# Performance work log

Hardware: AMD Instinct MI355X
Metric: run time of the kernel (lower is better)

## Reference

```python
import jax, jax.numpy as jnp
from jax import lax
import numpy as np

B, CB, HW, HID, P, NC = 128, 200, 32, 32, 4, 10
DEPTH, D, DI, DS, DR, K = 4, 128, 256, 16, 8, 4
G = HW // P                  # 8 -> 64 spatial patches
SPA_N = G * G
SPE_N = CB // 2              # 100 spectral patches
HS, HE = HW // 2 - 5 // 2, HW // 2 + 5 // 2 + 1   # centered 5x5 spectral crop: 14:19


def _sincos_1d(d, pos):
    omega = 1.0 / 10000 ** (np.arange(d // 2, dtype=np.float64) / (d / 2.0))
    out = np.outer(pos.reshape(-1).astype(np.float64), omega)
    return np.concatenate([np.sin(out), np.cos(out)], axis=1)


def _spa_pos_embed():
    # MAE get_2d_sincos_pos_embed with cls_token=True (zeros row FIRST)
    gw, gh = np.meshgrid(np.arange(G, dtype=np.float64), np.arange(G, dtype=np.float64))
    emb = np.concatenate([_sincos_1d(D // 2, gw), _sincos_1d(D // 2, gh)], axis=1)
    return np.concatenate([np.zeros((1, D)), emb], axis=0)  # (SPA_N+1, D)


def _spe_pos_embed():
    pe = np.zeros((SPE_N + 1, D))
    pos = np.arange(SPE_N + 1, dtype=np.float64)[:, None]
    div = np.exp(np.arange(0, D, 2) * -(np.log(10000.0) / D))
    pe[:, 0::2] = np.sin(pos * div)
    pe[:, 1::2] = np.cos(pos * div)
    return pe


def setup_inputs():
    keys = iter(jax.random.split(jax.random.key(0), 64))
    r = lambda shape, s=0.02: jax.random.normal(next(keys), shape, jnp.float32) * s
    return dict(
        x=jax.random.normal(next(keys), (B, CB, HW, HW), jnp.float32),
        spa_pos=jnp.asarray(_spa_pos_embed(), jnp.float32),
        spe_pos=jnp.asarray(_spe_pos_embed(), jnp.float32),
        dr_w1=r((HID, CB)), dr_b1=r((HID,)), bn1_g=1.0 + r((HID,)), bn1_b=r((HID,)),
        dr_w2=r((HID, HID)), dr_b2=r((HID,)), bn2_g=1.0 + r((HID,)), bn2_b=r((HID,)),
        spa_pw=r((D, HID, P, P)), spa_pb=r((D,)),
        spe_pw=r((D, 25, 2)), spe_pb=r((D,)),
        spa_cls=r((1, 1, D)), spe_cls=r((1, 1, D)),
        ln_g=jnp.ones((DEPTH, 2, D), jnp.float32), ln_b=jnp.zeros((DEPTH, 2, D), jnp.float32),
        in_w=r((DEPTH, 2, 2 * DI, D)),
        conv_w=r((DEPTH, 2, DI, K), 0.2), conv_b=r((DEPTH, 2, DI)),
        xp_w=r((DEPTH, 2, DR + 2 * DS, DI)),
        dtp_w=r((DEPTH, 2, DI, DR), 0.1), dtp_b=r((DEPTH, 2, DI), 0.1),
        a_log=jnp.log(jnp.tile(jnp.arange(1.0, DS + 1.0, dtype=jnp.float32), (DEPTH, 2, DI, 1))),
        d_p=jnp.ones((DEPTH, 2, DI), jnp.float32),
        out_w=r((DEPTH, 2, D, DI)),
        l1_w=r((DEPTH, D, D)),
        head_w=r((NC, D)), head_b=r((NC,)),
    )


def _layernorm(x, g, b, eps=1e-6):
    m = x.mean(-1, keepdims=True)
    v = jnp.mean((x - m) ** 2, axis=-1, keepdims=True)
    return (x - m) * lax.rsqrt(v + eps) * g + b


def _batchnorm(x, g, b, eps=1e-5):
    # training-mode BN: biased batch stats over (B,H,W) per channel
    m = x.mean((0, 2, 3), keepdims=True)
    v = x.var((0, 2, 3), keepdims=True)
    return (x - m) * lax.rsqrt(v + eps) * g[None, :, None, None] + b[None, :, None, None]


def _ssm(x, in_w, cw, cb, xpw, dtw, dtb, alog, dpar, ow):
    # standard Mamba selective-scan block (expand=2, d_conv=4)
    Bb, L, _ = x.shape
    xz = jnp.einsum('bld,ed->ble', x, in_w)
    xc, z = jnp.split(xz, 2, axis=-1)
    xt = jnp.pad(xc.transpose(0, 2, 1), ((0, 0), (0, 0), (K - 1, 0)))  # causal pad
    xt = lax.conv_general_dilated(xt, cw[:, None, :], (1,), 'VALID', feature_group_count=DI)
    xc = jax.nn.silu(xt + cb[None, :, None]).transpose(0, 2, 1)        # (B,L,DI)
    dbl = jnp.einsum('bld,ed->ble', xc, xpw)
    dt = jax.nn.softplus(jnp.einsum('blr,dr->bld', dbl[..., :DR], dtw) + dtb)
    Bm, Cm = dbl[..., DR:DR + DS], dbl[..., DR + DS:]
    dA = jnp.exp(dt[..., None] * (-jnp.exp(alog)))                     # (B,L,DI,DS)
    dBx = (dt * xc)[..., None] * Bm[:, :, None, :]                     # (B,L,DI,DS)

    def step(h, ab):
        h = ab[0] * h + ab[1]
        return h, h

    _, hs = lax.scan(step, jnp.zeros((Bb, DI, DS), xc.dtype),
                     (dA.transpose(1, 0, 2, 3), dBx.transpose(1, 0, 2, 3)))
    y = jnp.einsum('lbds,bls->bld', hs, Cm) + xc * dpar
    return jnp.einsum('bld,ed->ble', y * jax.nn.silu(z), ow)


def _block(inp, lg, lb, sp):
    # block_1D: bidirectional SSM with trailing cls token kept in place
    xn = _layernorm(inp, lg, lb)
    x1 = _ssm(xn, *sp)
    x2 = jnp.concatenate([xn[:, :-1][:, ::-1], xn[:, -1:]], axis=1)
    x3 = _ssm(x2, *sp)
    x3 = jnp.concatenate([x3[:, :-1][:, ::-1], x3[:, -1:]], axis=1)
    return (x1 + x3) * 0.5 + inp


def reference(x, spa_pos, spe_pos, dr_w1, dr_b1, bn1_g, bn1_b, dr_w2, dr_b2, bn2_g, bn2_b,
              spa_pw, spa_pb, spe_pw, spe_pb, spa_cls, spe_cls, ln_g, ln_b, in_w, conv_w,
              conv_b, xp_w, dtp_w, dtp_b, a_log, d_p, out_w, l1_w, head_w, head_b):
    Bb = x.shape[0]
    # dimen_redu: 1x1 conv -> BN -> ReLU -> 1x1 conv -> BN
    h = jnp.einsum('bchw,oc->bohw', x, dr_w1) + dr_b1[None, :, None, None]
    h = jax.nn.relu(_batchnorm(h, bn1_g, bn1_b))
    h = jnp.einsum('bchw,oc->bohw', h, dr_w2) + dr_b2[None, :, None, None]
    h = _batchnorm(h, bn2_g, bn2_b)
    # spatial patch embed (conv k=stride=P == patchify + matmul)
    hr = h.reshape(Bb, HID, G, P, G, P)
    x_spa = jnp.einsum('bcipjq,dcpq->bijd', hr, spa_pw).reshape(Bb, SPA_N, D) + spa_pb
    x_spa = x_spa + spa_pos[None, :-1, :]
    x_spa = jnp.concatenate([x_spa, jnp.broadcast_to(spa_cls + spa_pos[None, -1:, :], (Bb, 1, D))], axis=1)
    # spectral patch embed on centered 5x5 crop: Conv1d(25->D, k=stride=2) over bands
    xc = x[:, :, HS:HE, HS:HE].reshape(Bb, CB, 25).transpose(0, 2, 1).reshape(Bb, 25, SPE_N, 2)
    x_spe = jnp.einsum('bcls,dcs->bld', xc, spe_pw) + spe_pb
    x_spe = x_spe + spe_pos[None, :-1, :]
    x_spe = jnp.concatenate([x_spe, jnp.broadcast_to(spe_cls + spe_pos[None, -1:, :], (Bb, 1, D))], axis=1)
    for i in range(DEPTH):
        spa_p = (in_w[i, 0], conv_w[i, 0], conv_b[i, 0], xp_w[i, 0], dtp_w[i, 0], dtp_b[i, 0], a_log[i, 0], d_p[i, 0], out_w[i, 0])
        spe_p = (in_w[i, 1], conv_w[i, 1], conv_b[i, 1], xp_w[i, 1], dtp_w[i, 1], dtp_b[i, 1], a_log[i, 1], d_p[i, 1], out_w[i, 1])
        x_spa = _block(x_spa, ln_g[i, 0], ln_b[i, 0], spa_p)
        x_spe = _block(x_spe, ln_g[i, 1], ln_b[i, 1], spe_p)
        # sigmoid-gated fusion (fu=True)
        c = (x_spa[:, (x_spa.shape[1] - 1) // 2, :] + x_spe.mean(axis=1)) * 0.5
        sig = jax.nn.sigmoid(c @ l1_w[i].T)[:, None, :]
        x_spa = x_spa * sig
        x_spe = x_spe * sig
    out = (x_spa[:, -1] + x_spe[:, -1]) * 0.5   # cls tokens (global_pool=False)
    return out @ head_w.T + head_b
```

## Files before the change

### kernel.cpp

```cpp
#include <hip/hip_runtime.h>
#include <math.h>

typedef float4 f4;
typedef __attribute__((ext_vector_type(8))) short short8v;
typedef __attribute__((ext_vector_type(4))) float f32x4;
typedef __attribute__((ext_vector_type(2))) float f32x2;

constexpr int B_ = 128, CB_ = 200, HW_ = 32, HID_ = 32, D_ = 128, DI_ = 256;
constexpr int DS_ = 16, DR_ = 8, KC_ = 4, DEPTH_ = 4, NC_ = 10;
constexpr int LSPA_ = 65, LSPE_ = 101, NPIX_ = 1024;
constexpr int M1_ = B_ * NPIX_;
constexpr int NWI_ = DEPTH_*2*512*D_;
constexpr int NWO_ = DEPTH_*2*D_*DI_;
constexpr int NWX_ = DEPTH_*2*40*DI_;
constexpr int NWTR_ = 65536;

constexpr size_t O_XSPA = 0;
constexpr size_t O_XSPE = O_XSPA + (size_t)B_*LSPA_*D_;
constexpr size_t O_SC   = O_XSPE + (size_t)B_*LSPE_*D_;
constexpr size_t O_BN1P = O_SC + 512;
constexpr size_t O_BN2P = O_BN1P + 512*64;
constexpr size_t O_U    = O_BN2P + 512*64;
constexpr size_t O_HP1  = O_U;
constexpr size_t O_HP2  = O_U + (size_t)M1_*HID_;
constexpr size_t O_WTR  = O_HP2 + (size_t)M1_*HID_;
constexpr size_t O_XZSPA = O_U;
constexpr size_t O_XZSPE = O_XZSPA + (size_t)B_*LSPA_*512;
constexpr size_t O_XCSPA = O_XZSPE + (size_t)B_*LSPE_*512;
constexpr size_t O_XCSPE = O_XCSPA + (size_t)2*B_*LSPA_*DI_;
constexpr size_t O_DBSPA = O_XCSPE + (size_t)2*B_*LSPE_*DI_;
constexpr size_t O_DBSPE = O_DBSPA + (size_t)2*B_*LSPA_*40;
constexpr size_t O_YZSPA = O_DBSPE + (size_t)2*B_*LSPE_*40;
constexpr size_t O_YZSPE = O_YZSPA + (size_t)2*B_*LSPA_*DI_;
constexpr size_t O_WHI_I = O_YZSPE + (size_t)2*B_*LSPE_*DI_;
constexpr size_t O_WLO_I = O_WHI_I + NWI_/2;
constexpr size_t O_WHI_O = O_WLO_I + NWI_/2;
constexpr size_t O_WLO_O = O_WHI_O + NWO_/2;
constexpr size_t O_WHI_X = O_WLO_O + NWO_/2;
constexpr size_t O_WLO_X = O_WHI_X + NWX_/2;

static __device__ __forceinline__ unsigned short f2bf(float f) {
    unsigned int u = __float_as_uint(f);
    unsigned int r = u + 0x7fffu + ((u >> 16) & 1u);
    return (unsigned short)(r >> 16);
}
static __device__ __forceinline__ float bf2f(unsigned short h) {
    return __uint_as_float(((unsigned int)h) << 16);
}

__global__ __launch_bounds__(256) void k_stem1(const float* __restrict__ x,
        const float* __restrict__ w1, const float* __restrict__ b1,
        float* __restrict__ hpre1, float* __restrict__ part)
{
    __shared__ float smem[8448];
    float* sw = smem;
    const int t = threadIdx.x;
    for (int i = t; i < CB_*HID_; i += 256) {
        int c = i >> 5, o = i & 31;
        sw[i] = w1[o*CB_ + c];
    }
    const int m = blockIdx.x*256 + t;
    const int b = m >> 10, pix = m & 1023;
    const float* xp = x + (size_t)b*CB_*NPIX_ + pix;
    float h[HID_];
    #pragma unroll
    for (int o = 0; o < HID_; o++) h[o] = b1[o];
    __syncthreads();
    for (int c8 = 0; c8 < CB_; c8 += 8) {
        float xv[8];
        #pragma unroll
        for (int j = 0; j < 8; j++) xv[j] = xp[(size_t)(c8 + j)*NPIX_];
        #pragma unroll
        for (int j = 0; j < 8; j++) {
            const f4* wr = (const f4*)(sw + (c8 + j)*HID_);
            #pragma unroll
            for (int o8 = 0; o8 < 8; o8++) {
                f4 wv = wr[o8];
                h[o8*4+0] = fmaf(xv[j], wv.x, h[o8*4+0]);
                h[o8*4+1] = fmaf(xv[j], wv.y, h[o8*4+1]);
                h[o8*4+2] = fmaf(xv[j], wv.z, h[o8*4+2]);
                h[o8*4+3] = fmaf(xv[j], wv.w, h[o8*4+3]);
            }
        }
    }
    f4* hp = (f4*)(hpre1 + (size_t)m*HID_);
    #pragma unroll
    for (int o = 0; o < HID_; o += 4) { f4 v = {h[o],h[o+1],h[o+2],h[o+3]}; hp[o>>2] = v; }
    __syncthreads();
    float* sred = smem;
    #pragma unroll
    for (int o = 0; o < HID_; o++) sred[t*33 + o] = h[o];
    __syncthreads();
    if (t < HID_) {
        float s = 0.f, q = 0.f;
        for (int j = 0; j < 256; j++) { float v = sred[j*33 + t]; s += v; q += v*v; }
        part[blockIdx.x*64 + t]      = s;
        part[blockIdx.x*64 + 32 + t] = q;
    }
}

__global__ void k_bnfix(const float* __restrict__ part, const float* __restrict__ g,
        const float* __restrict__ bta, float* __restrict__ scale, float* __restrict__ shift)
{
    const int o = threadIdx.x;
    if (o >= 32) return;
    float s = 0.f, q = 0.f;
    for (int j = 0; j < 512; j++) { s += part[j*64 + o]; q += part[j*64 + 32 + o]; }
    const float mean = s / (float)M1_;
    const float var  = q / (float)M1_ - mean*mean;
    const float sc = g[o] * rsqrtf(var + 1e-5f);
    scale[o] = sc;
    shift[o] = bta[o] - mean*sc;
}

__global__ void k_bnfix_spa(const float* __restrict__ part, const float* __restrict__ g,
        const float* __restrict__ bta, const float* __restrict__ spa_pw,
        const float* __restrict__ spa_pb, float* __restrict__ scale,
        float* __restrict__ shift, float* __restrict__ spa_shift)
{
    __shared__ float ssh[32];
    const int t = threadIdx.x;
    if (t < 32) {
        float s = 0.f, q = 0.f;
        for (int j = 0; j < 512; j++) { s += part[j*64 + t]; q += part[j*64 + 32 + t]; }
        const float mean = s / (float)M1_;
        const float var  = q / (float)M1_ - mean*mean;
        const float sc = g[t] * rsqrtf(var + 1e-5f);
        scale[t] = sc;
        const float sh = bta[t] - mean*sc;
        shift[t] = sh;
        ssh[t] = sh;
    }
    __syncthreads();
    float acc = spa_pb[t];
    for (int c = 0; c < HID_; c++) {
        float wsum = 0.f;
        #pragma unroll
        for (int pq = 0; pq < 16; pq++) wsum += spa_pw[((size_t)t*HID_ + c)*16 + pq];
        acc = fmaf(ssh[c], wsum, acc);
    }
    spa_shift[t] = acc;
}

__global__ __launch_bounds__(256) void k_stem2(const float* __restrict__ hpre1,
        const float* __restrict__ w2, const float* __restrict__ b2,
        const float* __restrict__ sc1, const float* __restrict__ sh1,
        float* __restrict__ hpre2, float* __restrict__ part)
{
    __shared__ float smem[8448];
    __shared__ float s_sc[HID_], s_sh[HID_], s_b2[HID_];
    float* sw = smem;
    const int t = threadIdx.x;
    for (int i = t; i < HID_*HID_; i += 256) {
        int c = i >> 5, o = i & 31;
        sw[i] = w2[o*HID_ + c];
    }
    if (t < HID_) { s_sc[t] = sc1[t]; s_sh[t] = sh1[t]; s_b2[t] = b2[t]; }
    __syncthreads();
    const int m = blockIdx.x*256 + t;
    const f4* hp = (const f4*)(hpre1 + (size_t)m*HID_);
    float a[HID_];
    #pragma unroll
    for (int c = 0; c < HID_; c += 4) { f4 v = hp[c>>2]; a[c]=v.x; a[c+1]=v.y; a[c+2]=v.z; a[c+3]=v.w; }
    #pragma unroll
    for (int c = 0; c < HID_; c++) a[c] = fmaxf(fmaf(a[c], s_sc[c], s_sh[c]), 0.f);
    float h[HID_];
    #pragma unroll
    for (int o = 0; o < HID_; o++) h[o] = s_b2[o];
    #pragma unroll
    for (int c = 0; c < HID_; c++) {
        const f4* wr = (const f4*)(sw + c*HID_);
        #pragma unroll
        for (int o8 = 0; o8 < 8; o8++) {
            f4 wv = wr[o8];
            h[o8*4+0] = fmaf(a[c], wv.x, h[o8*4+0]);
            h[o8*4+1] = fmaf(a[c], wv.y, h[o8*4+1]);
            h[o8*4+2] = fmaf(a[c], wv.z, h[o8*4+2]);
            h[o8*4+3] = fmaf(a[c], wv.w, h[o8*4+3]);
        }
    }
    f4* op = (f4*)(hpre2 + (size_t)m*HID_);
    #pragma unroll
    for (int o = 0; o < HID_; o += 4) { f4 v = {h[o],h[o+1],h[o+2],h[o+3]}; op[o>>2] = v; }
    __syncthreads();
    float* sred = smem;
    #pragma unroll
    for (int o = 0; o < HID_; o++) sred[t*33 + o] = h[o];
    __syncthreads();
    if (t < HID_) {
        float s = 0.f, q = 0.f;
// ... 46 lines not shown
    for (int i = 0; i < 2; i++)
        #pragma unroll
        for (int j = 0; j < 8; j++) acc[i][j] = 0.f;
    for (int pq = 0; pq < 16; pq++) {
        const int p = pq >> 2, q = pq & 3;
        __syncthreads();
        for (int idx = t; idx < 32*8; idx += 256) {
            const int n = idx >> 3, c4 = (idx & 7)*4;
            const int nn = n0 + n;
            const int ii = nn >> 3, jj = nn & 7;
            const int pix = (ii*4 + p)*HW_ + jj*4 + q;
            f4 v = *(const f4*)(hpre2 + ((size_t)b*NPIX_ + pix)*HID_ + c4);
            float* pp = &sA[n*36 + c4];
            pp[0] = v.x*s_sc[c4]; pp[1] = v.y*s_sc[c4+1]; pp[2] = v.z*s_sc[c4+2]; pp[3] = v.w*s_sc[c4+3];
        }
        for (int idx = t; idx < 128*8; idx += 256) {
            const int dd = idx >> 3, c4 = (idx & 7)*4;
            f4 v = *(const f4*)(wtr + pq*4096 + dd*HID_ + c4);
            float* pp = &sB[dd*36 + c4];
            pp[0]=v.x; pp[1]=v.y; pp[2]=v.z; pp[3]=v.w;
        }
        __syncthreads();
        #pragma unroll
        for (int kq = 0; kq < 8; kq++) {
            f4 a0 = *(const f4*)&sA[(ty*2+0)*36 + kq*4];
            f4 a1 = *(const f4*)&sA[(ty*2+1)*36 + kq*4];
            #pragma unroll
            for (int j = 0; j < 8; j++) {
                const f4 bv = *(const f4*)&sB[(tx + 16*j)*36 + kq*4];
                acc[0][j] = fmaf(a0.x,bv.x,fmaf(a0.y,bv.y,fmaf(a0.z,bv.z,fmaf(a0.w,bv.w,acc[0][j]))));
                acc[1][j] = fmaf(a1.x,bv.x,fmaf(a1.y,bv.y,fmaf(a1.z,bv.z,fmaf(a1.w,bv.w,acc[1][j]))));
            }
        }
    }
    #pragma unroll
    for (int i = 0; i < 2; i++) {
        const int n = n0 + ty*2 + i;
        float* orow = xspa + ((size_t)b*LSPA_ + n)*D_;
        #pragma unroll
        for (int j = 0; j < 8; j++) {
            const int d = tx + 16*j;
            orow[d] = acc[i][j] + spa_shift[d] + spa_pos[n*D_ + d];
        }
    }
    if (half == 0 && t < D_)
        xspa[((size_t)b*LSPA_ + 64)*D_ + t] = spa_cls[t] + spa_pos[64*D_ + t];
}

__global__ __launch_bounds__(256) void k_spe(const float* __restrict__ x,
        const float* __restrict__ spe_pw, const float* __restrict__ spe_pb,
        const float* __restrict__ spe_pos, const float* __restrict__ spe_cls,
        float* __restrict__ xspe)
{
    const int b = blockIdx.x >> 1, half = blockIdx.x & 1;
    __shared__ float sx[100*25];
    __shared__ float sw[D_*51];
    const int t = threadIdx.x;
    for (int idx = t; idx < 100*25; idx += 256) {
        const int ch = idx / 25 + half*100, c = idx % 25;
        sx[idx] = x[(size_t)b*CB_*NPIX_ + (size_t)ch*NPIX_ + (14 + c/5)*HW_ + 14 + c%5];
    }
    for (int idx = t; idx < D_*50; idx += 256) sw[(idx/50)*51 + idx%50] = spe_pw[idx];
    __syncthreads();
    const int d = t & 127, ls = t >> 7;
    for (int j = ls; j < 50; j += 2) {
        const int l = half*50 + j;
        float acc = spe_pb[d];
        const float* wr = sw + d*51;
        const float* xr = sx + (2*j)*25;
        #pragma unroll
        for (int c = 0; c < 25; c++) {
            acc = fmaf(xr[c],      wr[c*2],     acc);
            acc = fmaf(xr[25 + c], wr[c*2 + 1], acc);
        }
        xspe[((size_t)b*LSPE_ + l)*D_ + d] = acc + spe_pos[l*D_ + d];
    }
    if (half == 1 && t < D_)
        xspe[((size_t)b*LSPE_ + 100)*D_ + t] = spe_cls[t] + spe_pos[100*D_ + t];
}

__global__ __launch_bounds__(256) void k_ln_in(const float* __restrict__ xspa,
        const float* __restrict__ xspe, float* __restrict__ xz_spa, float* __restrict__ xz_spe,
        const unsigned short* __restrict__ whi, const unsigned short* __restrict__ wlo,
        const float* __restrict__ ln_g, const float* __restrict__ ln_b, int depth)
{
    const int br = blockIdx.z;
    const int L = br ? LSPE_ : LSPA_;
    const int M = B_ * L;
    const int m0 = blockIdx.x*64;
    if (m0 >= M) return;
    const float* X  = br ? xspe : xspa;
    float* XZ = br ? xz_spe : xz_spa;
    const size_t wb = ((size_t)depth*2 + br) * 512 * (size_t)D_;
    const unsigned short* WH = whi + wb;
    const unsigned short* WL = wlo + wb;
    const float* gg = ln_g + ((size_t)depth*2 + br)*D_;
    const float* bb = ln_b + ((size_t)depth*2 + br)*D_;

    __shared__ __align__(16) unsigned short sAhi[64*136];
    __shared__ __align__(16) unsigned short sAlo[64*136];
    __shared__ __align__(16) unsigned short sBhi[128*40];
    __shared__ __align__(16) unsigned short sBlo[128*40];
    __shared__ float sgb[256];

    const int t = threadIdx.x;
    sgb[t] = (t < 128) ? gg[t] : bb[t-128];

    {
        const int row = t >> 2, tq = t & 3;
        const float* xr = X + (size_t)(m0 + row)*D_ + tq*32;
        float v[32];
        #pragma unroll
        for (int j4 = 0; j4 < 8; j4++) {
            f4 u = *(const f4*)(xr + j4*4);
            v[j4*4] = u.x; v[j4*4+1] = u.y; v[j4*4+2] = u.z; v[j4*4+3] = u.w;
        }
        float s = 0.f, q = 0.f;
        #pragma unroll
        for (int j = 0; j < 32; j++) { s += v[j]; q += v[j]*v[j]; }
        s += __shfl_xor(s, 1); q += __shfl_xor(q, 1);
        s += __shfl_xor(s, 2); q += __shfl_xor(q, 2);
        const float mean = s * (1.f/128.f);
        const float rstd = rsqrtf(q*(1.f/128.f) - mean*mean + 1e-6f);
        __syncthreads();
        unsigned short uh[32], ul[32];
        #pragma unroll
        for (int j = 0; j < 32; j++) {
            const int k = tq*32 + j;
            const float w = (v[j] - mean)*rstd*sgb[k] + sgb[128 + k];
            const unsigned short h = f2bf(w);
            uh[j] = h;
            ul[j] = f2bf(w - bf2f(h));
        }
        #pragma unroll
        for (int j4 = 0; j4 < 8; j4++) {
            ushort4 a = {uh[j4*4], uh[j4*4+1], uh[j4*4+2], uh[j4*4+3]};
            ushort4 b = {ul[j4*4], ul[j4*4+1], ul[j4*4+2], ul[j4*4+3]};
            *(ushort4*)&sAhi[row*136 + tq*32 + j4*4] = a;
            *(ushort4*)&sAlo[row*136 + tq*32 + j4*4] = b;
        }
    }
    __syncthreads();

    const int n0 = blockIdx.y * 128;
    const int wv = t >> 6, l = t & 63;
    const int wm = wv >> 1, wn = wv & 1;
    const int lr = l & 15, lg = l >> 4;
    f32x4 acc[2][4];
    #pragma unroll
    for (int i = 0; i < 2; i++)
        #pragma unroll
        for (int j = 0; j < 4; j++) acc[i][j] = (f32x4){0.f,0.f,0.f,0.f};

    for (int kc = 0; kc < 4; kc++) {
        {
            const int n = t >> 1, off = (t & 1)*16;
            const size_t g = (size_t)(n0 + n)*D_ + kc*32 + off;
            const uint4* ph = (const uint4*)(WH + g);
            const uint4* pl = (const uint4*)(WL + g);
            uint4 h0 = ph[0], h1 = ph[1];
            uint4 l0 = pl[0], l1 = pl[1];
            uint4* dh = (uint4*)&sBhi[n*40 + off];
            uint4* dl = (uint4*)&sBlo[n*40 + off];
            dh[0] = h0; dh[1] = h1;
            dl[0] = l0; dl[1] = l1;
        }
        __syncthreads();
        short8v ah[2], al[2], bh[4], bl[4];
        #pragma unroll
        for (int i = 0; i < 2; i++) {
            const int ro = (wm*32 + i*16 + lr)*136 + kc*32 + lg*8;
            ah[i] = *(const short8v*)&sAhi[ro];
            al[i] = *(const short8v*)&sAlo[ro];
        }
        #pragma unroll
        for (int j = 0; j < 4; j++) {
            const int co = (wn*64 + j*16 + lr)*40 + lg*8;
            bh[j] = *(const short8v*)&sBhi[co];
            bl[j] = *(const short8v*)&sBlo[co];
        }
        #pragma unroll
        for (int i = 0; i < 2; i++)
            #pragma unroll
            for (int j = 0; j < 4; j++) {
                acc[i][j] = __builtin_amdgcn_mfma_f32_16x16x32_bf16(ah[i], bh[j], acc[i][j], 0, 0, 0);
                acc[i][j] = __builtin_amdgcn_mfma_f32_16x16x32_bf16(ah[i], bl[j], acc[i][j], 0, 0, 0);
                acc[i][j] = __builtin_amdgcn_mfma_f32_16x16x32_bf16(al[i], bh[j], acc[i][j], 0, 0, 0);
            }
        __syncthreads();
    }

    #pragma unroll
    for (int i = 0; i < 2; i++) {
        const int rbase = m0 + wm*32 + i*16 + lg*4;
        #pragma unroll
        for (int j = 0; j < 4; j++) {
            const int col = n0 + wn*64 + j*16 + lr;
            #pragma unroll
            for (int r = 0; r < 4; r++)
                XZ[(size_t)(rbase + r)*512 + col] = acc[i][j][r];
        }
    }
}

__global__ __launch_bounds__(256) void k_conv(const float* __restrict__ xz_spa,
        const float* __restrict__ xz_spe, float* __restrict__ xc_spa, float* __restrict__ xc_spe,
        const float* __restrict__ conv_w, const float* __restrict__ conv_b, int depth)
{
    const int br = blockIdx.z;
    const int L = br ? LSPE_ : LSPA_;
    const int nt = (L + 15) / 16;
    const int b = blockIdx.x % B_;
    const int tl = blockIdx.x / B_;
    if (tl >= nt) return;
    const int l0 = tl * 16;
    const int d = threadIdx.x;
    const float* XZ = (br ? xz_spe : xz_spa) + (size_t)b*L*512 + d;
    float* XC0 = (br ? xc_spe : xc_spa) + ((size_t)(0*B_ + b)*L)*DI_ + d;
    float* XC1 = (br ? xc_spe : xc_spa) + ((size_t)(1*B_ + b)*L)*DI_ + d;
    const size_t w = (size_t)depth*2 + br;
    const float* cw = conv_w + (w*DI_ + d)*KC_;
    const float cb = conv_b[w*DI_ + d];
// ... 184 lines not shown
    _Pragma("unroll")                                                         \
    for (int c_ = 0; c_ < 8; ++c_) {                                          \
        const int l_ = (J0) + c_;                                             \
        if (l_ < L) {                                                         \
            const float* dr = &sD[BUF][c_*40];                                \
            const f4 q0 = *(const f4*)(dr);                                   \
            const f4 q1 = *(const f4*)(dr + 4);                               \
            f32x2 r2 = (f32x2){q0.x,q0.y} * dtw2[0];                          \
            r2 = __builtin_elementwise_fma((f32x2){q0.z,q0.w}, dtw2[1], r2);  \
            r2 = __builtin_elementwise_fma((f32x2){q1.x,q1.y}, dtw2[2], r2);  \
            r2 = __builtin_elementwise_fma((f32x2){q1.z,q1.w}, dtw2[3], r2);  \
            const float raw = dtb + r2.x + r2.y;                              \
            const float er = __builtin_amdgcn_exp2f(raw * 1.4426950408889634f);\
            const float dt = (raw > 20.f) ? raw                               \
                : __log2f(1.f + er) * 0.6931471805599453f;                    \
            const float xcv = RX[c_], zv = RZ[c_];                            \
            const float c2 = dt * xcv;                                        \
            const float E1 = __builtin_amdgcn_exp2f(nA0 * dt);                \
            const float E2 = E1 * E1;                                         \
            const f4 B0=*(const f4*)(dr+8),  B1=*(const f4*)(dr+12);          \
            const f4 B2=*(const f4*)(dr+16), B3=*(const f4*)(dr+20);          \
            const f4 C0=*(const f4*)(dr+24), C1=*(const f4*)(dr+28);          \
            const f4 C2=*(const f4*)(dr+32), C3=*(const f4*)(dr+36);          \
            const f32x2 Bp[8] = {{B0.x,B0.y},{B0.z,B0.w},{B1.x,B1.y},{B1.z,B1.w},\
                                 {B2.x,B2.y},{B2.z,B2.w},{B3.x,B3.y},{B3.z,B3.w}};\
            const f32x2 Cp[8] = {{C0.x,C0.y},{C0.z,C0.w},{C1.x,C1.y},{C1.z,C1.w},\
                                 {C2.x,C2.y},{C2.z,C2.w},{C3.x,C3.y},{C3.z,C3.w}};\
            f32x2 e = (f32x2){E1, E2};                                        \
            const f32x2 estep = (f32x2){E2, E2};                              \
            const f32x2 c2v = (f32x2){c2, c2};                                \
            f32x2 y2 = (f32x2){0.f, 0.f};                                     \
            _Pragma("unroll")                                                 \
            for (int j_ = 0; j_ < 8; ++j_) {                                  \
                h2[j_] = __builtin_elementwise_fma(h2[j_], e, c2v*Bp[j_]);    \
                y2 = __builtin_elementwise_fma(h2[j_], Cp[j_], y2);           \
                e = e * estep;                                                \
            }                                                                 \
            const float y = y2.x + y2.y;                                      \
            const float yt = fmaf(xcv, dpv, y);                               \
            const float sg = __builtin_amdgcn_rcpf(                           \
                1.f + __builtin_amdgcn_exp2f(-zv * 1.4426950408889634f));     \
            const int ls_ = dir ? ((l_ == L-1) ? (L-1) : (L-2-l_)) : l_;      \
            YZ[(size_t)ls_*DI_ + t] = yt * (zv * sg);                         \
        }                                                                     \
    }                                                                         \
} while(0)

    const int nch = (L + 7) >> 3;
    LOADD(0);
    LOADX(0, rxA, rzA);
    WRITED(0);
    __syncthreads();
    int ck = 0;
    while (true) {
        {
            const int j0 = ck*8;
            const bool more = (ck + 1 < nch);
            if (more) { LOADD(j0 + 8); LOADX(j0 + 8, rxB, rzB); }
            SCAN_CHUNK(j0, 0, rxA, rzA);
            if (more) WRITED(1);
            __syncthreads();
            if (!more) break;
            ck++;
        }
        {
            const int j0 = ck*8;
            const bool more = (ck + 1 < nch);
            if (more) { LOADD(j0 + 8); LOADX(j0 + 8, rxA, rzA); }
            SCAN_CHUNK(j0, 1, rxB, rzB);
            if (more) WRITED(0);
            __syncthreads();
            if (!more) break;
            ck++;
        }
    }
#undef LOADD
#undef WRITED
#undef LOADX
#undef SCAN_CHUNK
}

__global__ __launch_bounds__(256) void k_out(float* __restrict__ xspa, float* __restrict__ xspe,
        const float* __restrict__ yz_spa, const float* __restrict__ yz_spe,
        const unsigned short* __restrict__ whiO, const unsigned short* __restrict__ wloO, int depth)
{
    const int br = blockIdx.z;
    const int L = br ? LSPE_ : LSPA_;
    const int M = B_ * L;
    const int m0 = blockIdx.x*64;
    if (m0 >= M) return;
    float* X = br ? xspe : xspa;
    const float* Y0 = br ? yz_spe : yz_spa;
    const float* Y1 = Y0 + (size_t)B_*L*DI_;
    const size_t wb = ((size_t)depth*2 + br) * (size_t)D_ * DI_;
    const unsigned short* WH = whiO + wb;
    const unsigned short* WL = wloO + wb;

    __shared__ __align__(16) unsigned short sAhi[64*40];
    __shared__ __align__(16) unsigned short sAlo[64*40];
    __shared__ __align__(16) unsigned short sBhi[128*40];
    __shared__ __align__(16) unsigned short sBlo[128*40];

    const int t = threadIdx.x;
    const int wv = t >> 6, l = t & 63;
    const int wm = wv >> 1, wn = wv & 1;
    const int lr = l & 15, lg = l >> 4;
    f32x4 acc[2][4];
    #pragma unroll
    for (int i = 0; i < 2; i++)
        #pragma unroll
        for (int j = 0; j < 4; j++) acc[i][j] = (f32x4){0.f,0.f,0.f,0.f};

    for (int kc = 0; kc < 8; kc++) {
        {
            const int r = t >> 2, q = t & 3;
            const size_t g = (size_t)(m0 + r)*DI_ + kc*32 + q*8;
            unsigned short uh[8], ul[8];
            #pragma unroll
            for (int j4 = 0; j4 < 2; j4++) {
                f4 u0 = *(const f4*)(Y0 + g + j4*4);
                f4 u1 = *(const f4*)(Y1 + g + j4*4);
                float vv[4] = {u0.x+u1.x, u0.y+u1.y, u0.z+u1.z, u0.w+u1.w};
                #pragma unroll
                for (int e = 0; e < 4; e++) {
                    const unsigned short hh = f2bf(vv[e]);
                    uh[j4*4+e] = hh;
                    ul[j4*4+e] = f2bf(vv[e] - bf2f(hh));
                }
            }
            #pragma unroll
            for (int j4 = 0; j4 < 2; j4++) {
                ushort4 a = {uh[j4*4], uh[j4*4+1], uh[j4*4+2], uh[j4*4+3]};
                ushort4 b = {ul[j4*4], ul[j4*4+1], ul[j4*4+2], ul[j4*4+3]};
                *(ushort4*)&sAhi[r*40 + q*8 + j4*4] = a;
                *(ushort4*)&sAlo[r*40 + q*8 + j4*4] = b;
            }
            const int n = t >> 1, off = (t & 1)*16;
            const size_t gb = (size_t)n*DI_ + kc*32 + off;
            uint4 h0 = *(const uint4*)(WH + gb);
            uint4 h1 = *(const uint4*)(WH + gb + 8);
            uint4 l0 = *(const uint4*)(WL + gb);
            uint4 l1 = *(const uint4*)(WL + gb + 8);
            uint4* dh = (uint4*)&sBhi[n*40 + off];
            uint4* dl = (uint4*)&sBlo[n*40 + off];
            dh[0] = h0; dh[1] = h1;
            dl[0] = l0; dl[1] = l1;
        }
        __syncthreads();
        short8v ah[2], al[2], bh[4], bl[4];
        #pragma unroll
        for (int i = 0; i < 2; i++) {
            const int ro = (wm*32 + i*16 + lr)*40 + lg*8;
            ah[i] = *(const short8v*)&sAhi[ro];
            al[i] = *(const short8v*)&sAlo[ro];
        }
        #pragma unroll
        for (int j = 0; j < 4; j++) {
            const int co = (wn*64 + j*16 + lr)*40 + lg*8;
            bh[j] = *(const short8v*)&sBhi[co];
            bl[j] = *(const short8v*)&sBlo[co];
        }
        #pragma unroll
        for (int i = 0; i < 2; i++)
            #pragma unroll
            for (int j = 0; j < 4; j++) {
                acc[i][j] = __builtin_amdgcn_mfma_f32_16x16x32_bf16(ah[i], bh[j], acc[i][j], 0, 0, 0);
                acc[i][j] = __builtin_amdgcn_mfma_f32_16x16x32_bf16(ah[i], bl[j], acc[i][j], 0, 0, 0);
                acc[i][j] = __builtin_amdgcn_mfma_f32_16x16x32_bf16(al[i], bh[j], acc[i][j], 0, 0, 0);
            }
        __syncthreads();
    }

    #pragma unroll
    for (int i = 0; i < 2; i++) {
        const int rbase = m0 + wm*32 + i*16 + lg*4;
        #pragma unroll
        for (int j = 0; j < 4; j++) {
            const int col = wn*64 + j*16 + lr;
            #pragma unroll
            for (int r = 0; r < 4; r++)
                X[(size_t)(rbase + r)*D_ + col] += 0.5f*acc[i][j][r];
        }
    }
}

__global__ __launch_bounds__(256) void k_gate(float* __restrict__ xspa,
        float* __restrict__ xspe, const float* __restrict__ l1_w, int depth)
{
    __shared__ float sp[2][128];
    __shared__ float sc[128];
    __shared__ float sduo[256];
    __shared__ __align__(16) float ss[128];
    const int b = blockIdx.x, t = threadIdx.x;
    const int dd = t & 127, rh = t >> 7;
    float s = 0.f;
    for (int l = rh; l < LSPE_; l += 2) s += xspe[((size_t)b*LSPE_ + l)*D_ + dd];
    sp[rh][dd] = s;
    __syncthreads();
    if (t < 128)
        sc[t] = 0.5f*(xspa[((size_t)b*LSPA_ + 32)*D_ + t] + (sp[0][t]+sp[1][t])*(1.f/101.f));
    __syncthreads();
    {
        const float* wr = l1_w + (size_t)depth*D_*D_ + (size_t)dd*D_ + rh*64;
        float acc = 0.f;
        #pragma unroll 4
        for (int k = 0; k < 64; k++) acc = fmaf(sc[rh*64 + k], wr[k], acc);
        sduo[t] = acc;
    }
    __syncthreads();
    if (t < 128)
        ss[t] = 1.f/(1.f + __expf(-(sduo[t] + sduo[t+128])));
    __syncthreads();
    f4* pa = (f4*)(xspa + (size_t)b*LSPA_*D_);
    for (int idx = t; idx < LSPA_*32; idx += 256) {
        const f4 sg = *((const f4*)ss + (idx & 31));
        f4 v = pa[idx];
        v.x *= sg.x; v.y *= sg.y; v.z *= sg.z; v.w *= sg.w;
        pa[idx] = v;
    }
    f4* pe = (f4*)(xspe + (size_t)b*LSPE_*D_);
    for (int idx = t; idx < LSPE_*32; idx += 256) {
        const f4 sg = *((const f4*)ss + (idx & 31));
        f4 v = pe[idx];
        v.x *= sg.x; v.y *= sg.y; v.z *= sg.z; v.w *= sg.w;
        pe[idx] = v;
    }
}

__global__ void k_head(const float* __restrict__ xspa, const float* __restrict__ xspe,
        const float* __restrict__ head_w, const float* __restrict__ head_b, float* __restrict__ out)
{
    __shared__ float sv[D_];
    const int b = blockIdx.x, t = threadIdx.x;
    if (t < D_) sv[t] = 0.5f*(xspa[((size_t)b*LSPA_ + 64)*D_ + t] + xspe[((size_t)b*LSPE_ + 100)*D_ + t]);
    __syncthreads();
    if (t < NC_) {
        float acc = head_b[t];
        for (int k = 0; k < D_; k++) acc = fmaf(sv[k], head_w[t*D_ + k], acc);
        out[b*NC_ + t] = acc;
    }
}

extern "C" void kernel_launch(void* const* d_in, const int* in_sizes, int n_in,
                              void* d_out, int out_size, void* d_ws, size_t ws_size,
                              hipStream_t stream)
{
    const float* x       = (const float*)d_in[0];
    const float* spa_pos = (const float*)d_in[1];
    const float* spe_pos = (const float*)d_in[2];
    const float* dr_w1   = (const float*)d_in[3];
    const float* dr_b1   = (const float*)d_in[4];
    const float* bn1_g   = (const float*)d_in[5];
    const float* bn1_b   = (const float*)d_in[6];
    const float* dr_w2   = (const float*)d_in[7];
    const float* dr_b2   = (const float*)d_in[8];
    const float* bn2_g   = (const float*)d_in[9];
    const float* bn2_b   = (const float*)d_in[10];
    const float* spa_pw  = (const float*)d_in[11];
    const float* spa_pb  = (const float*)d_in[12];
    const float* spe_pw  = (const float*)d_in[13];
    const float* spe_pb  = (const float*)d_in[14];
    const float* spa_cls = (const float*)d_in[15];
    const float* spe_cls = (const float*)d_in[16];
    const float* ln_g    = (const float*)d_in[17];
    const float* ln_b    = (const float*)d_in[18];
    const float* in_w    = (const float*)d_in[19];
    const float* conv_w  = (const float*)d_in[20];
    const float* conv_b  = (const float*)d_in[21];
    const float* xp_w    = (const float*)d_in[22];
    const float* dtp_w   = (const float*)d_in[23];
    const float* dtp_b   = (const float*)d_in[24];
    const float* a_log   = (const float*)d_in[25];
    const float* d_p     = (const float*)d_in[26];
    const float* out_w   = (const float*)d_in[27];
    const float* l1_w    = (const float*)d_in[28];
    const float* head_w  = (const float*)d_in[29];
    const float* head_b  = (const float*)d_in[30];

    float* ws = (float*)d_ws;
    float* xspa   = ws + O_XSPA;
    float* xspe   = ws + O_XSPE;
    float* scale1 = ws + O_SC;
    float* shift1 = ws + O_SC + 32;
    float* scale2 = ws + O_SC + 64;
    float* shift2 = ws + O_SC + 96;
    float* spa_sh = ws + O_SC + 128;
    float* bn1p   = ws + O_BN1P;
    float* bn2p   = ws + O_BN2P;
    float* hpre1  = ws + O_HP1;
    float* hpre2  = ws + O_HP2;
    float* wtr    = ws + O_WTR;
    float* xz_spa = ws + O_XZSPA;
    float* xz_spe = ws + O_XZSPE;
    float* xc_spa = ws + O_XCSPA;
    float* xc_spe = ws + O_XCSPE;
    float* db_spa = ws + O_DBSPA;
    float* db_spe = ws + O_DBSPE;
    float* yz_spa = ws + O_YZSPA;
    float* yz_spe = ws + O_YZSPE;
    unsigned short* whiI = (unsigned short*)(ws + O_WHI_I);
    unsigned short* wloI = (unsigned short*)(ws + O_WLO_I);
    unsigned short* whiO = (unsigned short*)(ws + O_WHI_O);
    unsigned short* wloO = (unsigned short*)(ws + O_WLO_O);
    unsigned short* whiX = (unsigned short*)(ws + O_WHI_X);
    unsigned short* wloX = (unsigned short*)(ws + O_WLO_X);

    hipLaunchKernelGGL(k_stem1, dim3(512), dim3(256), 0, stream, x, dr_w1, dr_b1, hpre1, bn1p);
    hipLaunchKernelGGL(k_bnfix, dim3(1), dim3(32), 0, stream, bn1p, bn1_g, bn1_b, scale1, shift1);
    hipLaunchKernelGGL(k_wsplit, dim3((NWI_+NWO_+NWX_+NWTR_+255)/256), dim3(256), 0, stream,
                       in_w, out_w, xp_w, spa_pw, whiI, wloI, whiO, wloO, whiX, wloX, wtr);
    hipLaunchKernelGGL(k_stem2, dim3(512), dim3(256), 0, stream, hpre1, dr_w2, dr_b2, scale1, shift1, hpre2, bn2p);
    hipLaunchKernelGGL(k_bnfix_spa, dim3(1), dim3(128), 0, stream, bn2p, bn2_g, bn2_b,
                       spa_pw, spa_pb, scale2, shift2, spa_sh);
    hipLaunchKernelGGL(k_patch, dim3(256), dim3(256), 0, stream, hpre2, wtr, scale2, spa_sh, spa_pos, spa_cls, xspa);
    hipLaunchKernelGGL(k_spe, dim3(256), dim3(256), 0, stream, x, spe_pw, spe_pb, spe_pos, spe_cls, xspe);

    for (int i = 0; i < DEPTH_; i++) {
        hipLaunchKernelGGL(k_ln_in, dim3(202, 4, 2), dim3(256), 0, stream,
                           xspa, xspe, xz_spa, xz_spe, whiI, wloI, ln_g, ln_b, i);
        hipLaunchKernelGGL(k_conv, dim3(B_*7, 1, 2), dim3(256), 0, stream,
                           xz_spa, xz_spe, xc_spa, xc_spe, conv_w, conv_b, i);
        hipLaunchKernelGGL(k_xp, dim3(202, 1, 2), dim3(256), 0, stream,
                           xc_spa, xc_spe, db_spa, db_spe, whiX, wloX, i);
        hipLaunchKernelGGL(k_scan, dim3(B_, 2, 2), dim3(256), 0, stream,
                           xz_spa, xz_spe, xc_spa, xc_spe, db_spa, db_spe,
                           yz_spa, yz_spe, a_log, dtp_w, dtp_b, d_p, i);
        hipLaunchKernelGGL(k_out, dim3(202, 1, 2), dim3(256), 0, stream,
                           xspa, xspe, yz_spa, yz_spe, whiO, wloO, i);
        hipLaunchKernelGGL(k_gate, dim3(128), dim3(256), 0, stream, xspa, xspe, l1_w, i);
    }
    hipLaunchKernelGGL(k_head, dim3(128), dim3(128), 0, stream,
                       xspa, xspe, head_w, head_b, (float*)d_out);
}
```

Before: 711.9 us.

## Use split-bf16 MFMA in stem GEMM and fold sigmoid gating into consumers

The first stem 1x1-conv GEMM moves from per-thread fp32 FMAs to MFMA bf16 hi/lo split products. It now uses 128-row tiles and twice as many blocks, with a two-level in-block BN partial reduction. The per-depth gate kernel no longer rescales the whole spatial and spectral activations. It only writes the sigmoid vector, and the scale is applied lazily where the activations are next read: the LN/in-proj prologue, the out-proj residual update, and the head. This removes a full read-modify-write pass over the activations per depth and raises matrix throughput in the stem. In exchange it adds per-row division to find the batch index and slightly reduces precision in the stem GEMM.

```diff
diff --git a/kernel.cpp b/kernel.cpp
--- a/kernel.cpp
+++ b/kernel.cpp
@@ -19,7 +19,7 @@
 constexpr size_t O_XSPE = O_XSPA + (size_t)B_*LSPA_*D_;
 constexpr size_t O_SC   = O_XSPE + (size_t)B_*LSPE_*D_;
 constexpr size_t O_BN1P = O_SC + 512;
-constexpr size_t O_BN2P = O_BN1P + 512*64;
+constexpr size_t O_BN2P = O_BN1P + 1024*64;
 constexpr size_t O_U    = O_BN2P + 512*64;
 constexpr size_t O_HP1  = O_U;
 constexpr size_t O_HP2  = O_U + (size_t)M1_*HID_;
@@ -52,48 +52,108 @@
         const float* __restrict__ w1, const float* __restrict__ b1,
         float* __restrict__ hpre1, float* __restrict__ part)
 {
-    __shared__ float smem[8448];
-    float* sw = smem;
+    __shared__ __align__(16) unsigned char smem[25600];
+    unsigned short* sAhi = (unsigned short*)smem;
+    unsigned short* sAlo = (unsigned short*)(smem + 10240);
+    unsigned short* sBhi = (unsigned short*)(smem + 20480);
+    unsigned short* sBlo = (unsigned short*)(smem + 23040);
     const int t = threadIdx.x;
-    for (int i = t; i < CB_*HID_; i += 256) {
-        int c = i >> 5, o = i & 31;
-        sw[i] = w1[o*CB_ + c];
-    }
-    const int m = blockIdx.x*256 + t;
-    const int b = m >> 10, pix = m & 1023;
-    const float* xp = x + (size_t)b*CB_*NPIX_ + pix;
-    float h[HID_];
-    #pragma unroll
-    for (int o = 0; o < HID_; o++) h[o] = b1[o];
-    __syncthreads();
-    for (int c8 = 0; c8 < CB_; c8 += 8) {
-        float xv[8];
-        #pragma unroll
-        for (int j = 0; j < 8; j++) xv[j] = xp[(size_t)(c8 + j)*NPIX_];
-        #pragma unroll
-        for (int j = 0; j < 8; j++) {
-            const f4* wr = (const f4*)(sw + (c8 + j)*HID_);
-            #pragma unroll
-            for (int o8 = 0; o8 < 8; o8++) {
-                f4 wv = wr[o8];
-                h[o8*4+0] = fmaf(xv[j], wv.x, h[o8*4+0]);
-                h[o8*4+1] = fmaf(xv[j], wv.y, h[o8*4+1]);
-                h[o8*4+2] = fmaf(xv[j], wv.z, h[o8*4+2]);
-                h[o8*4+3] = fmaf(xv[j], wv.w, h[o8*4+3]);
-            }
-        }
-    }
-    f4* hp = (f4*)(hpre1 + (size_t)m*HID_);
-    #pragma unroll
-    for (int o = 0; o < HID_; o += 4) { f4 v = {h[o],h[o+1],h[o+2],h[o+3]}; hp[o>>2] = v; }
-    __syncthreads();
-    float* sred = smem;
-    #pragma unroll
-    for (int o = 0; o < HID_; o++) sred[t*33 + o] = h[o];
-    __syncthreads();
-    if (t < HID_) {
+    const int m0 = blockIdx.x * 128;
+    const int b = m0 >> 10, pix0 = m0 & 1023;
+    const float* xb = x + (size_t)b*CB_*NPIX_ + pix0;
+    const int wv = t >> 6, l = t & 63;
+    const int lr = l & 15, lg = l >> 4;
+    f32x4 acc[2][2];
+    #pragma unroll
+    for (int i = 0; i < 2; i++)
+        #pragma unroll
+        for (int j = 0; j < 2; j++) acc[i][j] = (f32x4){0.f,0.f,0.f,0.f};
+
+    const int rA = t >> 1, khA = (t & 1)*16;
+    for (int kc = 0; kc < 7; kc++) {
+        {
+            unsigned short uh[16], ul[16];
+            #pragma unroll
+            for (int j = 0; j < 16; j++) {
+                const int k = kc*32 + khA + j;
+                const float v = (k < CB_) ? xb[(size_t)k*NPIX_ + rA] : 0.f;
+                const unsigned short h = f2bf(v);
+                uh[j] = h; ul[j] = f2bf(v - bf2f(h));
+            }
+            #pragma unroll
+            for (int j4 = 0; j4 < 4; j4++) {
+                ushort4 a = {uh[j4*4], uh[j4*4+1], uh[j4*4+2], uh[j4*4+3]};
+                ushort4 c = {ul[j4*4], ul[j4*4+1], ul[j4*4+2], ul[j4*4+3]};
+                *(ushort4*)&sAhi[rA*40 + khA + j4*4] = a;
+                *(ushort4*)&sAlo[rA*40 + khA + j4*4] = c;
+            }
+            for (int idx = t; idx < 32*32; idx += 256) {
+                const int n = idx >> 5, kk = idx & 31;
+                const int k = kc*32 + kk;
+                const float v = (k < CB_) ? w1[n*CB_ + k] : 0.f;
+                const unsigned short h = f2bf(v);
+                sBhi[n*40 + kk] = h;
+                sBlo[n*40 + kk] = f2bf(v - bf2f(h));
+            }
+        }
+        __syncthreads();
+        short8v ah[2], al[2], bh[2], bl[2];
+        #pragma unroll
+        for (int i = 0; i < 2; i++) {
+            const int ro = (wv*32 + i*16 + lr)*40 + lg*8;
+            ah[i] = *(const short8v*)&sAhi[ro];
+            al[i] = *(const short8v*)&sAlo[ro];
+        }
+        #pragma unroll
+        for (int j = 0; j < 2; j++) {
+            const int co = (j*16 + lr)*40 + lg*8;
+            bh[j] = *(const short8v*)&sBhi[co];
+            bl[j] = *(const short8v*)&sBlo[co];
+        }
+        #pragma unroll
+        for (int i = 0; i < 2; i++)
+            #pragma unroll
+            for (int j = 0; j < 2; j++) {
+                acc[i][j] = __builtin_amdgcn_mfma_f32_16x16x32_bf16(ah[i], bh[j], acc[i][j], 0, 0, 0);
+                acc[i][j] = __builtin_amdgcn_mfma_f32_16x16x32_bf16(ah[i], bl[j], acc[i][j], 0, 0, 0);
+                acc[i][j] = __builtin_amdgcn_mfma_f32_16x16x32_bf16(al[i], bh[j], acc[i][j], 0, 0, 0);
+            }
+        __syncthreads();
+    }
+
+    float* sred = (float*)smem;
+    float* scomb = (float*)(smem + 20480);
+    #pragma unroll
+    for (int i = 0; i < 2; i++)
+        #pragma unroll
+        for (int j = 0; j < 2; j++) {
+            const int col = j*16 + lr;
+            const float bv = b1[col];
+            #pragma unroll
+            for (int r4 = 0; r4 < 4; r4++) {
+                const int row = wv*32 + i*16 + lg*4 + r4;
+                const float v = acc[i][j][r4] + bv;
+                hpre1[(size_t)(m0 + row)*HID_ + col] = v;
+                sred[row*33 + col] = v;
+            }
+        }
+    __syncthreads();
+    {
+        const int col = t & 31, grp = t >> 5;
         float s = 0.f, q = 0.f;
-        for (int j = 0; j < 256; j++) { float v = sred[j*33 + t]; s += v; q += v*v; }
+        #pragma unroll
+        for (int rr = 0; rr < 16; rr++) {
+            const float v = sred[(grp*16 + rr)*33 + col];
+            s += v; q += v*v;
+        }
+        scomb[grp*64 + col]      = s;
+        scomb[grp*64 + 32 + col] = q;
+    }
+    __syncthreads();
+    if (t < 32) {
+        float s = 0.f, q = 0.f;
+        #pragma unroll
+        for (int g = 0; g < 8; g++) { s += scomb[g*64 + t]; q += scomb[g*64 + 32 + t]; }
         part[blockIdx.x*64 + t]      = s;
         part[blockIdx.x*64 + 32 + t] = q;
     }
@@ -105,7 +165,7 @@
     const int o = threadIdx.x;
     if (o >= 32) return;
     float s = 0.f, q = 0.f;
-    for (int j = 0; j < 512; j++) { s += part[j*64 + o]; q += part[j*64 + 32 + o]; }
+    for (int j = 0; j < 1024; j++) { s += part[j*64 + o]; q += part[j*64 + 32 + o]; }
     const float mean = s / (float)M1_;
     const float var  = q / (float)M1_ - mean*mean;
     const float sc = g[o] * rsqrtf(var + 1e-5f);
@@ -318,7 +378,8 @@
 __global__ __launch_bounds__(256) void k_ln_in(const float* __restrict__ xspa,
         const float* __restrict__ xspe, float* __restrict__ xz_spa, float* __restrict__ xz_spe,
         const unsigned short* __restrict__ whi, const unsigned short* __restrict__ wlo,
-        const float* __restrict__ ln_g, const float* __restrict__ ln_b, int depth)
+        const float* __restrict__ ln_g, const float* __restrict__ ln_b,
+        const float* __restrict__ sig, int depth)
 {
     const int br = blockIdx.z;
     const int L = br ? LSPE_ : LSPA_;
@@ -344,12 +405,23 @@
 
     {
         const int row = t >> 2, tq = t & 3;
-        const float* xr = X + (size_t)(m0 + row)*D_ + tq*32;
+        const int grow = m0 + row;
+        const int b = grow / L;
+        const float* xr = X + (size_t)grow*D_ + tq*32;
         float v[32];
         #pragma unroll
         for (int j4 = 0; j4 < 8; j4++) {
             f4 u = *(const f4*)(xr + j4*4);
             v[j4*4] = u.x; v[j4*4+1] = u.y; v[j4*4+2] = u.z; v[j4*4+3] = u.w;
+        }
+        if (depth > 0) {
+            const float* sgp = sig + (size_t)b*D_ + tq*32;
+            #pragma unroll
+            for (int j4 = 0; j4 < 8; j4++) {
+                f4 u = *(const f4*)(sgp + j4*4);
+                v[j4*4]   *= u.x; v[j4*4+1] *= u.y;
+                v[j4*4+2] *= u.z; v[j4*4+3] *= u.w;
+            }
         }
         float s = 0.f, q = 0.f;
         #pragma unroll
@@ -371,9 +443,9 @@
         #pragma unroll
         for (int j4 = 0; j4 < 8; j4++) {
             ushort4 a = {uh[j4*4], uh[j4*4+1], uh[j4*4+2], uh[j4*4+3]};
-            ushort4 b = {ul[j4*4], ul[j4*4+1], ul[j4*4+2], ul[j4*4+3]};
+            ushort4 b2 = {ul[j4*4], ul[j4*4+1], ul[j4*4+2], ul[j4*4+3]};
             *(ushort4*)&sAhi[row*136 + tq*32 + j4*4] = a;
-            *(ushort4*)&sAlo[row*136 + tq*32 + j4*4] = b;
+            *(ushort4*)&sAlo[row*136 + tq*32 + j4*4] = b2;
         }
     }
     __syncthreads();
@@ -724,7 +796,8 @@
 
 __global__ __launch_bounds__(256) void k_out(float* __restrict__ xspa, float* __restrict__ xspe,
         const float* __restrict__ yz_spa, const float* __restrict__ yz_spe,
-        const unsigned short* __restrict__ whiO, const unsigned short* __restrict__ wloO, int depth)
+        const unsigned short* __restrict__ whiO, const unsigned short* __restrict__ wloO,
+        const float* __restrict__ sig, int depth)
 {
     const int br = blockIdx.z;
     const int L = br ? LSPE_ : LSPA_;
@@ -815,24 +888,29 @@
 
     #pragma unroll
     for (int i = 0; i < 2; i++) {
-        const int rbase = m0 + wm*32 + i*16 + lg*4;
-        #pragma unroll
-        for (int j = 0; j < 4; j++) {
-            const int col = wn*64 + j*16 + lr;
-            #pragma unroll
-            for (int r = 0; r < 4; r++)
-                X[(size_t)(rbase + r)*D_ + col] += 0.5f*acc[i][j][r];
-        }
-    }
-}
-
-__global__ __launch_bounds__(256) void k_gate(float* __restrict__ xspa,
-        float* __restrict__ xspe, const float* __restrict__ l1_w, int depth)
+        #pragma unroll
+        for (int r = 0; r < 4; r++) {
+            const int rowg = m0 + wm*32 + i*16 + lg*4 + r;
+            const int b = rowg / L;
+            const float* sgp = sig + (size_t)b*D_;
+            #pragma unroll
+            for (int j = 0; j < 4; j++) {
+                const int col = wn*64 + j*16 + lr;
+                float* xp = X + (size_t)rowg*D_ + col;
+                const float sgv = (depth > 0) ? sgp[col] : 1.f;
+                *xp = fmaf(sgv, *xp, 0.5f*acc[i][j][r]);
+            }
+        }
+    }
+}
+
+__global__ __launch_bounds__(256) void k_sig(const float* __restrict__ xspa,
+        const float* __restrict__ xspe, const float* __restrict__ l1_w,
+        float* __restrict__ sig, int depth)
 {
     __shared__ float sp[2][128];
     __shared__ float sc[128];
     __shared__ float sduo[256];
-    __shared__ __align__(16) float ss[128];
     const int b = blockIdx.x, t = threadIdx.x;
     const int dd = t & 127, rh = t >> 7;
     float s = 0.f;
@@ -851,30 +929,19 @@
     }
     __syncthreads();
     if (t < 128)
-        ss[t] = 1.f/(1.f + __expf(-(sduo[t] + sduo[t+128])));
-    __syncthreads();
-    f4* pa = (f4*)(xspa + (size_t)b*LSPA_*D_);
-    for (int idx = t; idx < LSPA_*32; idx += 256) {
-        const f4 sg = *((const f4*)ss + (idx & 31));
-        f4 v = pa[idx];
-        v.x *= sg.x; v.y *= sg.y; v.z *= sg.z; v.w *= sg.w;
-        pa[idx] = v;
-    }
-    f4* pe = (f4*)(xspe + (size_t)b*LSPE_*D_);
-    for (int idx = t; idx < LSPE_*32; idx += 256) {
-        const f4 sg = *((const f4*)ss + (idx & 31));
-        f4 v = pe[idx];
-        v.x *= sg.x; v.y *= sg.y; v.z *= sg.z; v.w *= sg.w;
-        pe[idx] = v;
-    }
+        sig[(size_t)b*D_ + t] = 1.f/(1.f + __expf(-(sduo[t] + sduo[t+128])));
 }
 
 __global__ void k_head(const float* __restrict__ xspa, const float* __restrict__ xspe,
-        const float* __restrict__ head_w, const float* __restrict__ head_b, float* __restrict__ out)
+        const float* __restrict__ head_w, const float* __restrict__ head_b,
+        const float* __restrict__ sig, float* __restrict__ out)
 {
     __shared__ float sv[D_];
     const int b = blockIdx.x, t = threadIdx.x;
-    if (t < D_) sv[t] = 0.5f*(xspa[((size_t)b*LSPA_ + 64)*D_ + t] + xspe[((size_t)b*LSPE_ + 100)*D_ + t]);
+    if (t < D_) {
+        const float sg = sig[(size_t)b*D_ + t];
+        sv[t] = 0.5f*(xspa[((size_t)b*LSPA_ + 64)*D_ + t]*sg + xspe[((size_t)b*LSPE_ + 100)*D_ + t]*sg);
+    }
     __syncthreads();
     if (t < NC_) {
         float acc = head_b[t];
@@ -929,6 +996,7 @@
     float* spa_sh = ws + O_SC + 128;
     float* bn1p   = ws + O_BN1P;
     float* bn2p   = ws + O_BN2P;
+    float* sigb   = ws + O_BN1P;
     float* hpre1  = ws + O_HP1;
     float* hpre2  = ws + O_HP2;
     float* wtr    = ws + O_WTR;
@@ -947,7 +1015,7 @@
     unsigned short* whiX = (unsigned short*)(ws + O_WHI_X);
     unsigned short* wloX = (unsigned short*)(ws + O_WLO_X);
 
-    hipLaunchKernelGGL(k_stem1, dim3(512), dim3(256), 0, stream, x, dr_w1, dr_b1, hpre1, bn1p);
+    hipLaunchKernelGGL(k_stem1, dim3(1024), dim3(256), 0, stream, x, dr_w1, dr_b1, hpre1, bn1p);
     hipLaunchKernelGGL(k_bnfix, dim3(1), dim3(32), 0, stream, bn1p, bn1_g, bn1_b, scale1, shift1);
     hipLaunchKernelGGL(k_wsplit, dim3((NWI_+NWO_+NWX_+NWTR_+255)/256), dim3(256), 0, stream,
                        in_w, out_w, xp_w, spa_pw, whiI, wloI, whiO, wloO, whiX, wloX, wtr);
@@ -959,7 +1027,7 @@
 
     for (int i = 0; i < DEPTH_; i++) {
         hipLaunchKernelGGL(k_ln_in, dim3(202, 4, 2), dim3(256), 0, stream,
-                           xspa, xspe, xz_spa, xz_spe, whiI, wloI, ln_g, ln_b, i);
+                           xspa, xspe, xz_spa, xz_spe, whiI, wloI, ln_g, ln_b, sigb, i);
         hipLaunchKernelGGL(k_conv, dim3(B_*7, 1, 2), dim3(256), 0, stream,
                            xz_spa, xz_spe, xc_spa, xc_spe, conv_w, conv_b, i);
         hipLaunchKernelGGL(k_xp, dim3(202, 1, 2), dim3(256), 0, stream,
@@ -968,9 +1036,9 @@
                            xz_spa, xz_spe, xc_spa, xc_spe, db_spa, db_spe,
                            yz_spa, yz_spe, a_log, dtp_w, dtp_b, d_p, i);
         hipLaunchKernelGGL(k_out, dim3(202, 1, 2), dim3(256), 0, stream,
-                           xspa, xspe, yz_spa, yz_spe, whiO, wloO, i);
-        hipLaunchKernelGGL(k_gate, dim3(128), dim3(256), 0, stream, xspa, xspe, l1_w, i);
+                           xspa, xspe, yz_spa, yz_spe, whiO, wloO, sigb, i);
+        hipLaunchKernelGGL(k_sig, dim3(128), dim3(256), 0, stream, xspa, xspe, l1_w, sigb, i);
     }
     hipLaunchKernelGGL(k_head, dim3(128), dim3(128), 0, stream,
-                       xspa, xspe, head_w, head_b, (float*)d_out);
-}
+                       xspa, xspe, head_w, head_b, sigb, (float*)d_out);
+}
```

Measured after the change: 718.5 us (median of 2 runs). Within noise of the previous version (+0.9%).
